# Kernel tuning notes

Measured on AMD Instinct MI355X. Metric: run time of the kernel, lower is better.

Reference implementation:

```python
import jax, jax.numpy as jnp
import numpy as np

IMG = 800.0
OUT = 7          # roi_size
SR = 2           # sampling_ratio per bin axis
STRIDES = (4, 8, 16)
N_CLASS = 21


def _make_rois(key, n):
    k1, k2, k3, k4 = jax.random.split(key, 4)
    cy = jax.random.uniform(k1, (n,), minval=100.0, maxval=700.0)
    cx = jax.random.uniform(k2, (n,), minval=100.0, maxval=700.0)
    # log-uniform sizes 32..448 px -> spans pyramid levels 2..4
    h = jnp.exp(jax.random.uniform(k3, (n,), minval=np.log(32.0), maxval=np.log(448.0)))
    w = jnp.exp(jax.random.uniform(k4, (n,), minval=np.log(32.0), maxval=np.log(448.0)))
    y1 = jnp.clip(cy - h / 2, 0.0, IMG - 2)
    x1 = jnp.clip(cx - w / 2, 0.0, IMG - 2)
    y2 = jnp.clip(cy + h / 2, y1 + 1.0, IMG - 1)
    x2 = jnp.clip(cx + w / 2, x1 + 1.0, IMG - 1)
    return jnp.stack([y1, x1, y2, x2], axis=1)  # [N,4] (y1,x1,y2,x2) as in source


def setup_inputs() -> dict:
    key = jax.random.key(0)
    ks = jax.random.split(key, 12)
    B, C, N = 2, 512, 512
    inp = {
        'feat2': jax.random.normal(ks[0], (B, C, 200, 200), jnp.float32),
        'feat3': jax.random.normal(ks[1], (B, C, 100, 100), jnp.float32),
        'feat4': jax.random.normal(ks[2], (B, C, 50, 50), jnp.float32),
        'rois': _make_rois(ks[3], N),
        'roi_indices': jax.random.randint(ks[4], (N,), 0, B, jnp.int32),
        'w_fc1': jax.random.normal(ks[5], (C * OUT * OUT, 4096), jnp.float32) * 0.01,
        'b_fc1': jnp.zeros((4096,), jnp.float32),
        'w_fc2': jax.random.normal(ks[6], (4096, 4096), jnp.float32) * 0.01,
        'b_fc2': jnp.zeros((4096,), jnp.float32),
        'w_loc': jax.random.normal(ks[7], (4096, N_CLASS * 4), jnp.float32) * 0.01,
        'b_loc': jnp.zeros((N_CLASS * 4,), jnp.float32),
        'w_score': jax.random.normal(ks[8], (4096, N_CLASS), jnp.float32) * 0.01,
        'b_score': jnp.zeros((N_CLASS,), jnp.float32),
    }
    return inp


def roi_align(feat, boxes, b_idx, scale):
    """feat [B,C,H,W]; boxes [N,4] x1,y1,x2,y2 in image coords -> [N,C,OUT,OUT]."""
    H, W = feat.shape[2], feat.shape[3]
    x1 = boxes[:, 0] * scale
    y1 = boxes[:, 1] * scale
    x2 = boxes[:, 2] * scale
    y2 = boxes[:, 3] * scale
    roi_w = jnp.maximum(x2 - x1, 1.0)
    roi_h = jnp.maximum(y2 - y1, 1.0)
    S = OUT * SR
    offs = (jnp.arange(S, dtype=feat.dtype) + 0.5) / (SR * OUT)  # fraction of roi extent
    ys = jnp.clip(y1[:, None] + roi_h[:, None] * offs, 0.0, H - 1.0)  # [N,S]
    xs = jnp.clip(x1[:, None] + roi_w[:, None] * offs, 0.0, W - 1.0)
    y0f = jnp.floor(ys); x0f = jnp.floor(xs)
    ly = ys - y0f; lx = xs - x0f
    y0 = y0f.astype(jnp.int32); x0 = x0f.astype(jnp.int32)
    y1i = jnp.minimum(y0 + 1, H - 1); x1i = jnp.minimum(x0 + 1, W - 1)
    b = b_idx[:, None, None]

    def g(yi, xi):  # -> [N,S,S,C]
        return feat[b, :, yi[:, :, None], xi[:, None, :]]

    wy0 = (1 - ly)[:, :, None, None]; wy1 = ly[:, :, None, None]
    wx0 = (1 - lx)[:, None, :, None]; wx1 = lx[:, None, :, None]
    val = (g(y0, x0) * wy0 * wx0 + g(y0, x1i) * wy0 * wx1
           + g(y1i, x0) * wy1 * wx0 + g(y1i, x1i) * wy1 * wx1)  # [N,S,S,C]
    N, C = boxes.shape[0], feat.shape[1]
    pooled = val.reshape(N, OUT, SR, OUT, SR, C).mean(axis=(2, 4))  # [N,OUT,OUT,C]
    return jnp.transpose(pooled, (0, 3, 1, 2))


def reference(feat2, feat3, feat4, rois, roi_indices, w_fc1, b_fc1, w_fc2, b_fc2,
              w_loc, b_loc, w_score, b_score):
    # pyramid level assignment (levels 2..4)
    roi_h = rois[:, 2] - rois[:, 0] + 1.0
    roi_w = rois[:, 3] - rois[:, 1] + 1.0
    lvl = jnp.round(jnp.log2(jnp.sqrt(roi_h * roi_w) / 224.0) + 4.0)
    lvl = jnp.clip(lvl, 2.0, 4.0).astype(jnp.int32)  # [N]

    boxes_xyxy = rois[:, jnp.array([1, 0, 3, 2])]  # (x1,y1,x2,y2)
    b_idx = roi_indices.astype(jnp.int32)

    p2 = roi_align(feat2, boxes_xyxy, b_idx, 1.0 / STRIDES[0])
    p3 = roi_align(feat3, boxes_xyxy, b_idx, 1.0 / STRIDES[1])
    p4 = roi_align(feat4, boxes_xyxy, b_idx, 1.0 / STRIDES[2])
    m = lvl[:, None, None, None]
    pooled = jnp.where(m == 2, p2, jnp.where(m == 3, p3, p4))  # [N,C,7,7]
    # (per-level split + sort-by-original-index in the source == original roi order)

    flat = pooled.reshape(pooled.shape[0], -1)  # [N, C*7*7]
    fc6 = jax.nn.relu(flat @ w_fc1 + b_fc1)
    fc7 = jax.nn.relu(fc6 @ w_fc2 + b_fc2)
    roi_cls_locs = fc7 @ w_loc + b_loc
    roi_scores = fc7 @ w_score + b_score
    return roi_cls_locs, roi_scores
```

## Files before the change

### kernel.cpp

```cpp
#include <hip/hip_runtime.h>
#include <hip/hip_bf16.h>

typedef __attribute__((ext_vector_type(4))) float  f32x4;
typedef __attribute__((ext_vector_type(2))) float  f32x2;
typedef __attribute__((ext_vector_type(4))) short  s16x4;
typedef __attribute__((ext_vector_type(8))) short  s16x8;
typedef __attribute__((ext_vector_type(8))) __bf16 v8bf;

__device__ __forceinline__ short f2bf(float f) {
    unsigned u = __builtin_bit_cast(unsigned, f);
    unsigned r = (u + 0x7fffu + ((u >> 16) & 1u)) >> 16;
    return (short)r;
}
__device__ __forceinline__ float bf2f(short s) {
    unsigned u = ((unsigned)(unsigned short)s) << 16;
    return __builtin_bit_cast(float, u);
}
__device__ __forceinline__ v8bf as_bf(s16x8 x) { return __builtin_bit_cast(v8bf, x); }

__global__ __launch_bounds__(256) void roi_pool_kernel(
    const float* __restrict__ feat2, const float* __restrict__ feat3,
    const float* __restrict__ feat4, const float* __restrict__ rois,
    const int* __restrict__ roi_idx, float* __restrict__ out) {
    const int r = blockIdx.x;
    const float y1r = rois[r*4+0], x1r = rois[r*4+1];
    const float y2r = rois[r*4+2], x2r = rois[r*4+3];
    const float rh = y2r - y1r + 1.0f, rw = x2r - x1r + 1.0f;
    float lvlf = rintf(log2f(sqrtf(rh*rw) / 224.0f) + 4.0f);
    lvlf = fminf(fmaxf(lvlf, 2.0f), 4.0f);
    const int lvl = (int)lvlf;
    const float* feat; int H; float scale;
    if (lvl == 2)      { feat = feat2; H = 200; scale = 0.25f;   }
    else if (lvl == 3) { feat = feat3; H = 100; scale = 0.125f;  }
    else               { feat = feat4; H = 50;  scale = 0.0625f; }
    const int W = H;
    const int b = roi_idx[r];

    const float x1 = x1r*scale, y1 = y1r*scale, x2 = x2r*scale, y2 = y2r*scale;
    const float roiw = fmaxf(x2 - x1, 1.0f), roih = fmaxf(y2 - y1, 1.0f);

    __shared__ int   sy0[14], sy1[14], sx0[14], sx1[14];
    __shared__ float sly[14], slx[14];
    const int t = threadIdx.x;
    if (t < 14) {
        float off = ((float)t + 0.5f) * (1.0f/14.0f);
        float ys = fminf(fmaxf(y1 + roih*off, 0.0f), (float)(H-1));
        float yf = floorf(ys);
        sy0[t] = (int)yf; sly[t] = ys - yf; sy1[t] = min((int)yf + 1, H-1);
    } else if (t < 28) {
        int j = t - 14;
        float off = ((float)j + 0.5f) * (1.0f/14.0f);
        float xs = fminf(fmaxf(x1 + roiw*off, 0.0f), (float)(W-1));
        float xf = floorf(xs);
        sx0[j] = (int)xf; slx[j] = xs - xf; sx1[j] = min((int)xf + 1, W-1);
    }
    __syncthreads();

    const float* fb = feat + (size_t)b * 512 * H * W;
    float* ob = out + (size_t)r * 25088;
    for (int idx = t; idx < 25088; idx += 256) {
        const int c = idx / 49, p = idx % 49;
        const int oy = p / 7, ox = p % 7;
        const float* fc = fb + (size_t)c * H * W;
        float acc = 0.0f;
        #pragma unroll
        for (int sy = 0; sy < 2; ++sy) {
            const int iy = oy*2 + sy;
            const int ya = sy0[iy], yb = sy1[iy];
            const float ly = sly[iy], wy0 = 1.0f - ly;
            const float* r0 = fc + (size_t)ya * W;
            const float* r1 = fc + (size_t)yb * W;
            #pragma unroll
            for (int sx = 0; sx < 2; ++sx) {
                const int ix = ox*2 + sx;
                const int xa = sx0[ix], xb = sx1[ix];
                const float lx = slx[ix], wx0 = 1.0f - lx;
                acc += r0[xa]*wy0*wx0 + r0[xb]*wy0*lx
                     + r1[xa]*ly*wx0  + r1[xb]*ly*lx;
            }
        }
        ob[idx] = acc * 0.25f;
    }
}

#define GKS 4
__global__ __launch_bounds__(512) void gemm_split_kernel(
    const float* __restrict__ A, const float* __restrict__ B,
    float* __restrict__ P, int K, int N, int ksub) {
    __shared__ unsigned short As_hi[4096], As_lo[4096], Bs_hi[4096], Bs_lo[4096];

    const int tid = threadIdx.x;
    const int m0 = blockIdx.y * 128;
    const int n0 = blockIdx.x * 128;
    const int k0base = blockIdx.z * ksub;
    const int nsteps = ksub >> 5;

    const int w    = tid >> 6;
    const int lane = tid & 63;
    const int wm   = w >> 1;
    const int wn   = w & 1;
    const int lr   = lane & 15;
    const int lg   = lane >> 4;

    f32x4 acc[2][4];
    #pragma unroll
    for (int i = 0; i < 2; ++i)
        #pragma unroll
        for (int j = 0; j < 4; ++j) acc[i][j] = f32x4{0.f, 0.f, 0.f, 0.f};

    const int a_m  = tid >> 3;
    const int a_kc = tid & 7;
    const int b_np = tid & 63;
    const int b_kq = tid >> 6;

    for (int step = 0; step < nsteps; ++step) {
        const int k0 = k0base + (step << 5);
        {
            const float* ap = A + (size_t)(m0 + a_m) * K + k0 + a_kc * 4;
            f32x4 v0 = *(const f32x4*)ap;
            f32x4 v1 = *(const f32x4*)(ap + (size_t)64 * K);
            const int kg = a_kc >> 1, sub0 = (a_kc & 1) * 4;
            const int e0 = (((kg << 10) + a_m * 8 + sub0) ^ (kg << 4));
            const int e1 = (((kg << 10) + (a_m + 64) * 8 + sub0) ^ (kg << 4));
            s16x4 h0, l0, h1, l1;
            #pragma unroll
            for (int j = 0; j < 4; ++j) {
                short h = f2bf(v0[j]); h0[j] = h; l0[j] = f2bf(v0[j] - bf2f(h));
                short g = f2bf(v1[j]); h1[j] = g; l1[j] = f2bf(v1[j] - bf2f(g));
            }
            *(s16x4*)(&As_hi[e0]) = h0; *(s16x4*)(&As_lo[e0]) = l0;
            *(s16x4*)(&As_hi[e1]) = h1; *(s16x4*)(&As_lo[e1]) = l1;
        }
        {
            const float* bp = B + (size_t)(k0 + b_kq * 4) * N + n0 + b_np * 2;
            f32x2 u0 = *(const f32x2*)bp;
            f32x2 u1 = *(const f32x2*)(bp + (size_t)N);
            f32x2 u2 = *(const f32x2*)(bp + (size_t)2 * N);
            f32x2 u3 = *(const f32x2*)(bp + (size_t)3 * N);
            const int kg = b_kq >> 1, sub0 = (b_kq & 1) * 4;
            #pragma unroll
            for (int e = 0; e < 2; ++e) {
                float vals[4] = {u0[e], u1[e], u2[e], u3[e]};
                s16x4 h, l;
                #pragma unroll
                for (int j = 0; j < 4; ++j) {
                    short hh = f2bf(vals[j]); h[j] = hh; l[j] = f2bf(vals[j] - bf2f(hh));
                }
                const int ei = (((kg << 10) + (b_np * 2 + e) * 8 + sub0) ^ (kg << 4));
                *(s16x4*)(&Bs_hi[ei]) = h; *(s16x4*)(&Bs_lo[ei]) = l;
            }
        }
        __syncthreads();
        s16x8 a_hi[2], a_lo[2];
        #pragma unroll
        for (int i = 0; i < 2; ++i) {
            const int m = wm * 32 + i * 16 + lr;
            const int e = (((lg << 10) + m * 8) ^ (lg << 4));
            a_hi[i] = *(const s16x8*)(&As_hi[e]);
            a_lo[i] = *(const s16x8*)(&As_lo[e]);
        }
        #pragma unroll
        for (int j = 0; j < 4; ++j) {
            const int n = wn * 64 + j * 16 + lr;
            const int e = (((lg << 10) + n * 8) ^ (lg << 4));
            v8bf b_hi = as_bf(*(const s16x8*)(&Bs_hi[e]));
            v8bf b_lo = as_bf(*(const s16x8*)(&Bs_lo[e]));
            #pragma unroll
            for (int i = 0; i < 2; ++i) {
                v8bf ah = as_bf(a_hi[i]), al = as_bf(a_lo[i]);
                acc[i][j] = __builtin_amdgcn_mfma_f32_16x16x32_bf16(ah, b_hi, acc[i][j], 0, 0, 0);
                acc[i][j] = __builtin_amdgcn_mfma_f32_16x16x32_bf16(ah, b_lo, acc[i][j], 0, 0, 0);
                acc[i][j] = __builtin_amdgcn_mfma_f32_16x16x32_bf16(al, b_hi, acc[i][j], 0, 0, 0);
            }
        }
        __syncthreads();
    }
    float* pb = P + (size_t)blockIdx.z * 512 * N;
    #pragma unroll
    for (int i = 0; i < 2; ++i)
        #pragma unroll
        for (int j = 0; j < 4; ++j) {
            const int gn = n0 + wn * 64 + j * 16 + lr;
            #pragma unroll
            for (int rr = 0; rr < 4; ++rr) {
                const int gm = m0 + wm * 32 + i * 16 + lg * 4 + rr;
                pb[(size_t)gm * N + gn] = acc[i][j][rr];
            }
        }
}

__global__ __launch_bounds__(256) void reduce_bias_relu(
    const float* __restrict__ P, const float* __restrict__ bias,
    float* __restrict__ out, int total, int N, int do_relu) {
    int i = (blockIdx.x * 256 + threadIdx.x) * 4;
    if (i >= total) return;
    f32x4 a0 = *(const f32x4*)(P + i);
    f32x4 a1 = *(const f32x4*)(P + (size_t)total + i);
    f32x4 a2 = *(const f32x4*)(P + (size_t)2 * total + i);
    f32x4 a3 = *(const f32x4*)(P + (size_t)3 * total + i);
    f32x4 bb = *(const f32x4*)(bias + (i % N));
    f32x4 r = (a0 + a1) + (a2 + a3) + bb;
    if (do_relu) {
        #pragma unroll
        for (int j = 0; j < 4; ++j) r[j] = fmaxf(r[j], 0.f);
    }
    *(f32x4*)(out + i) = r;
}

__global__ __launch_bounds__(128) void heads_kernel(
    const float* __restrict__ fc7,
    const float* __restrict__ w_loc, const float* __restrict__ b_loc,
    const float* __restrict__ w_score, const float* __restrict__ b_score,
    float* __restrict__ out, int nroi) {
    __shared__ float row[4096];
    const int r = blockIdx.x;
    const float* fr = fc7 + (size_t)r * 4096;
    for (int i = threadIdx.x; i < 4096; i += 128) row[i] = fr[i];
    __syncthreads();
    const int n = threadIdx.x;
    if (n < 84) {
        float s0 = 0.f, s1 = 0.f, s2 = 0.f, s3 = 0.f;
        for (int k = 0; k < 4096; k += 4) {
            s0 += row[k+0] * w_loc[(size_t)(k+0) * 84 + n];
            s1 += row[k+1] * w_loc[(size_t)(k+1) * 84 + n];
            s2 += row[k+2] * w_loc[(size_t)(k+2) * 84 + n];
            s3 += row[k+3] * w_loc[(size_t)(k+3) * 84 + n];
        }
        out[(size_t)r * 84 + n] = b_loc[n] + ((s0 + s1) + (s2 + s3));
    } else if (n < 105) {
        const int c = n - 84;
        float s0 = 0.f, s1 = 0.f, s2 = 0.f, s3 = 0.f;
        for (int k = 0; k < 4096; k += 4) {
            s0 += row[k+0] * w_score[(size_t)(k+0) * 21 + c];
            s1 += row[k+1] * w_score[(size_t)(k+1) * 21 + c];
            s2 += row[k+2] * w_score[(size_t)(k+2) * 21 + c];
            s3 += row[k+3] * w_score[(size_t)(k+3) * 21 + c];
        }
        out[(size_t)nroi * 84 + (size_t)r * 21 + c] = b_score[c] + ((s0 + s1) + (s2 + s3));
    }
}

extern "C" void kernel_launch(void* const* d_in, const int* in_sizes, int n_in,
                              void* d_out, int out_size, void* d_ws, size_t ws_size,
                              hipStream_t stream) {
    const float* feat2   = (const float*)d_in[0];
    const float* feat3   = (const float*)d_in[1];
    const float* feat4   = (const float*)d_in[2];
    const float* rois    = (const float*)d_in[3];
    const int*   roi_idx = (const int*)d_in[4];
    const float* w_fc1   = (const float*)d_in[5];
    const float* b_fc1   = (const float*)d_in[6];
    const float* w_fc2   = (const float*)d_in[7];
    const float* b_fc2   = (const float*)d_in[8];
    const float* w_loc   = (const float*)d_in[9];
    const float* b_loc   = (const float*)d_in[10];
    const float* w_score = (const float*)d_in[11];
    const float* b_score = (const float*)d_in[12];
    float* out = (float*)d_out;

    const int nroi = in_sizes[4];
    const int FDIM = 25088;
    const int HID  = 4096;

    char* ws = (char*)d_ws;
    const size_t off_flat = 0;
    const size_t off_part = 51380224;
    const size_t off_fc6  = off_part + 33554432;
    const size_t need     = off_fc6 + 8388608;
    if (ws_size < need) return;
    float* flat = (float*)(ws + off_flat);
    float* part = (float*)(ws + off_part);
    float* fc6  = (float*)(ws + off_fc6);
    float* fc7  = (float*)(ws + off_flat);

    roi_pool_kernel<<<nroi, 256, 0, stream>>>(feat2, feat3, feat4, rois, roi_idx, flat);

    gemm_split_kernel<<<dim3(HID/128, 512/128, GKS), 512, 0, stream>>>(
        flat, w_fc1, part, FDIM, HID, FDIM / GKS);
    reduce_bias_relu<<<(512 * HID / 4 + 255) / 256, 256, 0, stream>>>(
        part, b_fc1, fc6, 512 * HID, HID, 1);

    gemm_split_kernel<<<dim3(HID/128, 512/128, GKS), 512, 0, stream>>>(
        fc6, w_fc2, part, HID, HID, HID / GKS);
    reduce_bias_relu<<<(512 * HID / 4 + 255) / 256, 256, 0, stream>>>(
        part, b_fc2, fc7, 512 * HID, HID, 1);

    heads_kernel<<<nroi, 128, 0, stream>>>(fc7, w_loc, b_loc, w_score, b_score, out, nroi);
}
```

Baseline: 1.408 ms.

## Rewrite pipeline with pre-split bf16 activations, 256x256 double-buffered GEMM and atomic split-K

The ROI pool now writes activations already split into bf16 hi/lo planes in an MFMA-ready tiled layout, and the fc6 reduce does the same for the second GEMM. The GEMM uses 256x256 tiles with 8 K-splits and stages A into LDS directly via global_load_lds. It double-buffers A and B, overlaps the next B conversion with MFMAs, and accumulates split-K partials with atomicAdd into a zeroed buffer. The heads kernel splits K across two thread halves. These changes cut redundant A conversion and partial-buffer traffic, at the cost of fp32 atomics, which make the summation order nondeterministic, plus extra zeroing launches.

```diff
diff --git a/kernel.cpp b/kernel.cpp
--- a/kernel.cpp
+++ b/kernel.cpp
@@ -2,31 +2,35 @@
 #include <hip/hip_bf16.h>
 
 typedef __attribute__((ext_vector_type(4))) float  f32x4;
-typedef __attribute__((ext_vector_type(2))) float  f32x2;
-typedef __attribute__((ext_vector_type(4))) short  s16x4;
 typedef __attribute__((ext_vector_type(8))) short  s16x8;
 typedef __attribute__((ext_vector_type(8))) __bf16 v8bf;
 
-__device__ __forceinline__ short f2bf(float f) {
+__device__ __forceinline__ unsigned short f2bf_u(float f) {
     unsigned u = __builtin_bit_cast(unsigned, f);
     unsigned r = (u + 0x7fffu + ((u >> 16) & 1u)) >> 16;
-    return (short)r;
-}
-__device__ __forceinline__ float bf2f(short s) {
-    unsigned u = ((unsigned)(unsigned short)s) << 16;
+    return (unsigned short)r;
+}
+__device__ __forceinline__ float bfu2f(unsigned short s) {
+    unsigned u = ((unsigned)s) << 16;
     return __builtin_bit_cast(float, u);
 }
-__device__ __forceinline__ v8bf as_bf(s16x8 x) { return __builtin_bit_cast(v8bf, x); }
-
-__global__ __launch_bounds__(256) void roi_pool_kernel(
+
+__global__ __launch_bounds__(448) void roi_pool_split(
     const float* __restrict__ feat2, const float* __restrict__ feat3,
     const float* __restrict__ feat4, const float* __restrict__ rois,
-    const int* __restrict__ roi_idx, float* __restrict__ out) {
-    const int r = blockIdx.x;
+    const int* __restrict__ roi_idx,
+    unsigned short* __restrict__ Ah, unsigned short* __restrict__ Al) {
+    const int r  = blockIdx.x;
+    const int by = blockIdx.y;
+    const int t  = threadIdx.x;
+
+    __shared__ int   syA[14], syB[14], sxA[14], sxB[14];
+    __shared__ float sly[14], slx[14];
+    __shared__ float pool[3584];
+
     const float y1r = rois[r*4+0], x1r = rois[r*4+1];
     const float y2r = rois[r*4+2], x2r = rois[r*4+3];
-    const float rh = y2r - y1r + 1.0f, rw = x2r - x1r + 1.0f;
-    float lvlf = rintf(log2f(sqrtf(rh*rw) / 224.0f) + 4.0f);
+    float lvlf = rintf(log2f(sqrtf((y2r - y1r + 1.0f) * (x2r - x1r + 1.0f)) / 224.0f) + 4.0f);
     lvlf = fminf(fmaxf(lvlf, 2.0f), 4.0f);
     const int lvl = (int)lvlf;
     const float* feat; int H; float scale;
@@ -34,209 +38,281 @@
     else if (lvl == 3) { feat = feat3; H = 100; scale = 0.125f;  }
     else               { feat = feat4; H = 50;  scale = 0.0625f; }
     const int W = H;
-    const int b = roi_idx[r];
+    const int HW = H * W;
 
     const float x1 = x1r*scale, y1 = y1r*scale, x2 = x2r*scale, y2 = y2r*scale;
     const float roiw = fmaxf(x2 - x1, 1.0f), roih = fmaxf(y2 - y1, 1.0f);
 
-    __shared__ int   sy0[14], sy1[14], sx0[14], sx1[14];
-    __shared__ float sly[14], slx[14];
-    const int t = threadIdx.x;
     if (t < 14) {
         float off = ((float)t + 0.5f) * (1.0f/14.0f);
         float ys = fminf(fmaxf(y1 + roih*off, 0.0f), (float)(H-1));
         float yf = floorf(ys);
-        sy0[t] = (int)yf; sly[t] = ys - yf; sy1[t] = min((int)yf + 1, H-1);
+        int ya = (int)yf;
+        syA[t] = ya * W; sly[t] = ys - yf; syB[t] = min(ya + 1, H-1) * W;
     } else if (t < 28) {
         int j = t - 14;
         float off = ((float)j + 0.5f) * (1.0f/14.0f);
         float xs = fminf(fmaxf(x1 + roiw*off, 0.0f), (float)(W-1));
         float xf = floorf(xs);
-        sx0[j] = (int)xf; slx[j] = xs - xf; sx1[j] = min((int)xf + 1, W-1);
-    }
-    __syncthreads();
-
-    const float* fb = feat + (size_t)b * 512 * H * W;
-    float* ob = out + (size_t)r * 25088;
-    for (int idx = t; idx < 25088; idx += 256) {
-        const int c = idx / 49, p = idx % 49;
-        const int oy = p / 7, ox = p % 7;
-        const float* fc = fb + (size_t)c * H * W;
+        int xa = (int)xf;
+        sxA[j] = xa; slx[j] = xs - xf; sxB[j] = min(xa + 1, W-1);
+    }
+    __syncthreads();
+
+    const float* fb = feat + (size_t)roi_idx[r] * 512 * HW;
+    const int wv = t >> 6, lane = t & 63;
+
+    #pragma unroll
+    for (int j = 0; j < 8; ++j) {
+        const int kl = wv*512 + j*64 + lane;
+        const int kg = by*3584 + kl;
+        const int c  = kg / 49;
+        const int p  = kg - c*49;
+        const int oy = p / 7;
+        const int ox = p - oy*7;
+        const float* fc = fb + (size_t)c * HW;
         float acc = 0.0f;
         #pragma unroll
         for (int sy = 0; sy < 2; ++sy) {
             const int iy = oy*2 + sy;
-            const int ya = sy0[iy], yb = sy1[iy];
+            const int ra = syA[iy], rb = syB[iy];
             const float ly = sly[iy], wy0 = 1.0f - ly;
-            const float* r0 = fc + (size_t)ya * W;
-            const float* r1 = fc + (size_t)yb * W;
             #pragma unroll
             for (int sx = 0; sx < 2; ++sx) {
                 const int ix = ox*2 + sx;
-                const int xa = sx0[ix], xb = sx1[ix];
+                const int xa = sxA[ix], xb = sxB[ix];
                 const float lx = slx[ix], wx0 = 1.0f - lx;
-                acc += r0[xa]*wy0*wx0 + r0[xb]*wy0*lx
-                     + r1[xa]*ly*wx0  + r1[xb]*ly*lx;
+                acc += fc[ra+xa]*wy0*wx0 + fc[ra+xb]*wy0*lx
+                     + fc[rb+xa]*ly*wx0  + fc[rb+xb]*ly*lx;
             }
         }
-        ob[idx] = acc * 0.25f;
-    }
-}
-
-#define GKS 4
-__global__ __launch_bounds__(512) void gemm_split_kernel(
-    const float* __restrict__ A, const float* __restrict__ B,
-    float* __restrict__ P, int K, int N, int ksub) {
-    __shared__ unsigned short As_hi[4096], As_lo[4096], Bs_hi[4096], Bs_lo[4096];
-
-    const int tid = threadIdx.x;
-    const int m0 = blockIdx.y * 128;
-    const int n0 = blockIdx.x * 128;
-    const int k0base = blockIdx.z * ksub;
+        pool[kl] = acc * 0.25f;
+    }
+    __syncthreads();
+
+    const int k0l = t * 8;
+    const int k0  = by*3584 + k0l;
+    f32x4 v0 = *(const f32x4*)(&pool[k0l]);
+    f32x4 v1 = *(const f32x4*)(&pool[k0l+4]);
+    float v[8] = {v0[0],v0[1],v0[2],v0[3],v1[0],v1[1],v1[2],v1[3]};
+    s16x8 hi, lo;
+    #pragma unroll
+    for (int i = 0; i < 8; ++i) {
+        unsigned short h = f2bf_u(v[i]);
+        hi[i] = (short)h;
+        lo[i] = (short)f2bf_u(v[i] - bfu2f(h));
+    }
+    const int mb = r >> 4, row = r & 15;
+    const int kb = k0 >> 5, ko = (k0 >> 3) & 3;
+    const size_t off = ((((size_t)mb*784 + kb)*4 + ko)*16 + row)*8;
+    *(s16x8*)(Ah + off) = hi;
+    *(s16x8*)(Al + off) = lo;
+}
+
+__global__ __launch_bounds__(256) void zero_f32(float* __restrict__ p, int n4) {
+    int i = blockIdx.x*256 + threadIdx.x;
+    if (i < n4) ((f32x4*)p)[i] = f32x4{0.f,0.f,0.f,0.f};
+}
+
+__global__ __launch_bounds__(512, 2) void gemm_split3(
+    const unsigned short* __restrict__ Ah, const unsigned short* __restrict__ Al,
+    const float* __restrict__ B, float* __restrict__ P,
+    const int K, const int ksub) {
+    extern __shared__ char lds[];
+    const int tid  = threadIdx.x;
+    const int lane = tid & 63;
+    const int wv   = tid >> 6;
+    const int wm   = wv >> 2;
+    const int wn   = wv & 3;
+
+    int L = (int)blockIdx.x;
+    L = (L & 7) * 32 + (L >> 3);
+    const int mblk = L & 1;
+    const int nblk = (L >> 1) & 15;
+    const int zblk = L >> 5;
+    const int m0 = mblk * 256;
+    const int n0 = nblk * 256;
+    const int KB = K >> 5;
+    const int kb0 = (zblk * ksub) >> 5;
     const int nsteps = ksub >> 5;
 
-    const int w    = tid >> 6;
-    const int lane = tid & 63;
-    const int wm   = w >> 1;
-    const int wn   = w & 1;
-    const int lr   = lane & 15;
-    const int lg   = lane >> 4;
-
-    f32x4 acc[2][4];
-    #pragma unroll
-    for (int i = 0; i < 2; ++i)
-        #pragma unroll
-        for (int j = 0; j < 4; ++j) acc[i][j] = f32x4{0.f, 0.f, 0.f, 0.f};
-
-    const int a_m  = tid >> 3;
-    const int a_kc = tid & 7;
-    const int b_np = tid & 63;
-    const int b_kq = tid >> 6;
-
-    for (int step = 0; step < nsteps; ++step) {
-        const int k0 = k0base + (step << 5);
-        {
-            const float* ap = A + (size_t)(m0 + a_m) * K + k0 + a_kc * 4;
-            f32x4 v0 = *(const f32x4*)ap;
-            f32x4 v1 = *(const f32x4*)(ap + (size_t)64 * K);
-            const int kg = a_kc >> 1, sub0 = (a_kc & 1) * 4;
-            const int e0 = (((kg << 10) + a_m * 8 + sub0) ^ (kg << 4));
-            const int e1 = (((kg << 10) + (a_m + 64) * 8 + sub0) ^ (kg << 4));
-            s16x4 h0, l0, h1, l1;
+    const int b_col = tid & 15;
+    const int b_nb  = (tid >> 4) & 15;
+    const int b_kq  = tid >> 8;
+    const float* Bbase = B + (size_t)(n0 + b_nb*16 + b_col);
+
+    f32x4 acc[8][4];
+    #pragma unroll
+    for (int i = 0; i < 8; ++i)
+        #pragma unroll
+        for (int j = 0; j < 4; ++j) acc[i][j] = f32x4{0.f,0.f,0.f,0.f};
+
+    float bv[16];
+
+    auto loadB = [&](int kb) {
+        const float* bp = Bbase + (size_t)(kb*32 + b_kq*16) * 4096;
+        #pragma unroll
+        for (int i = 0; i < 16; ++i) bv[i] = bp[(size_t)i * 4096];
+    };
+    auto stageA = [&](int kb, char* buf) {
+        #pragma unroll
+        for (int c = 0; c < 4; ++c) {
+            const int ch = wv*4 + c;
+            const unsigned short* src = ((ch & 16) ? Al : Ah)
+                + ((size_t)((m0 >> 4) + (ch & 15)) * KB + kb) * 512 + lane*8;
+            char* dst = buf + (ch >> 4) * 16384 + (ch & 15) * 1024;
+            __builtin_amdgcn_global_load_lds((const void*)src, (void*)dst, 16, 0, 0);
+        }
+    };
+    auto convB = [&](char* buf) {
+        #pragma unroll
+        for (int o2 = 0; o2 < 2; ++o2) {
+            s16x8 hi, lo;
             #pragma unroll
-            for (int j = 0; j < 4; ++j) {
-                short h = f2bf(v0[j]); h0[j] = h; l0[j] = f2bf(v0[j] - bf2f(h));
-                short g = f2bf(v1[j]); h1[j] = g; l1[j] = f2bf(v1[j] - bf2f(g));
+            for (int i = 0; i < 8; ++i) {
+                float f = bv[o2*8 + i];
+                unsigned short h = f2bf_u(f);
+                hi[i] = (short)h;
+                lo[i] = (short)f2bf_u(f - bfu2f(h));
             }
-            *(s16x4*)(&As_hi[e0]) = h0; *(s16x4*)(&As_lo[e0]) = l0;
-            *(s16x4*)(&As_hi[e1]) = h1; *(s16x4*)(&As_lo[e1]) = l1;
-        }
-        {
-            const float* bp = B + (size_t)(k0 + b_kq * 4) * N + n0 + b_np * 2;
-            f32x2 u0 = *(const f32x2*)bp;
-            f32x2 u1 = *(const f32x2*)(bp + (size_t)N);
-            f32x2 u2 = *(const f32x2*)(bp + (size_t)2 * N);
-            f32x2 u3 = *(const f32x2*)(bp + (size_t)3 * N);
-            const int kg = b_kq >> 1, sub0 = (b_kq & 1) * 4;
+            const int oct = b_kq*2 + o2;
+            char* p = buf + 32768 + b_nb*1024 + oct*256 + b_col*16;
+            *(s16x8*)p = hi;
+            *(s16x8*)(p + 16384) = lo;
+        }
+    };
+    auto mfma_half = [&](int h, const char* buf) {
+        s16x8 ah[4], al[4];
+        #pragma unroll
+        for (int mf = 0; mf < 4; ++mf) {
+            const int ch = wm*8 + h*4 + mf;
+            ah[mf] = *(const s16x8*)(buf + ch*1024 + lane*16);
+            al[mf] = *(const s16x8*)(buf + 16384 + ch*1024 + lane*16);
+        }
+        #pragma unroll
+        for (int nf = 0; nf < 4; ++nf) {
+            const int nb = wn*4 + nf;
+            v8bf bh = __builtin_bit_cast(v8bf, *(const s16x8*)(buf + 32768 + nb*1024 + lane*16));
+            v8bf bl = __builtin_bit_cast(v8bf, *(const s16x8*)(buf + 49152 + nb*1024 + lane*16));
             #pragma unroll
-            for (int e = 0; e < 2; ++e) {
-                float vals[4] = {u0[e], u1[e], u2[e], u3[e]};
-                s16x4 h, l;
-                #pragma unroll
-                for (int j = 0; j < 4; ++j) {
-                    short hh = f2bf(vals[j]); h[j] = hh; l[j] = f2bf(vals[j] - bf2f(hh));
-                }
-                const int ei = (((kg << 10) + (b_np * 2 + e) * 8 + sub0) ^ (kg << 4));
-                *(s16x4*)(&Bs_hi[ei]) = h; *(s16x4*)(&Bs_lo[ei]) = l;
+            for (int mf = 0; mf < 4; ++mf) {
+                v8bf a1 = __builtin_bit_cast(v8bf, ah[mf]);
+                v8bf a2 = __builtin_bit_cast(v8bf, al[mf]);
+                const int mi = h*4 + mf;
+                acc[mi][nf] = __builtin_amdgcn_mfma_f32_16x16x32_bf16(a1, bh, acc[mi][nf], 0,0,0);
+                acc[mi][nf] = __builtin_amdgcn_mfma_f32_16x16x32_bf16(a1, bl, acc[mi][nf], 0,0,0);
+                acc[mi][nf] = __builtin_amdgcn_mfma_f32_16x16x32_bf16(a2, bh, acc[mi][nf], 0,0,0);
             }
         }
+    };
+
+    char* buf0 = lds;
+    char* buf1 = lds + 65536;
+
+    stageA(kb0, buf0);
+    loadB(kb0);
+    convB(buf0);
+    __syncthreads();
+
+    for (int s = 0; s < nsteps; ++s) {
+        char* cur = (s & 1) ? buf1 : buf0;
+        char* nxt = (s & 1) ? buf0 : buf1;
+        const bool more = (s + 1 < nsteps);
+        if (more) { stageA(kb0 + s + 1, nxt); loadB(kb0 + s + 1); }
+        mfma_half(0, cur);
+        if (more) convB(nxt);
+        mfma_half(1, cur);
         __syncthreads();
-        s16x8 a_hi[2], a_lo[2];
-        #pragma unroll
-        for (int i = 0; i < 2; ++i) {
-            const int m = wm * 32 + i * 16 + lr;
-            const int e = (((lg << 10) + m * 8) ^ (lg << 4));
-            a_hi[i] = *(const s16x8*)(&As_hi[e]);
-            a_lo[i] = *(const s16x8*)(&As_lo[e]);
-        }
-        #pragma unroll
-        for (int j = 0; j < 4; ++j) {
-            const int n = wn * 64 + j * 16 + lr;
-            const int e = (((lg << 10) + n * 8) ^ (lg << 4));
-            v8bf b_hi = as_bf(*(const s16x8*)(&Bs_hi[e]));
-            v8bf b_lo = as_bf(*(const s16x8*)(&Bs_lo[e]));
+    }
+
+    const int orow = (lane >> 4) * 4;
+    const int ocol = lane & 15;
+    #pragma unroll
+    for (int mi = 0; mi < 8; ++mi) {
+        const int gm = m0 + wm*128 + mi*16 + orow;
+        #pragma unroll
+        for (int nf = 0; nf < 4; ++nf) {
+            const int gn = n0 + wn*64 + nf*16 + ocol;
+            float* pp = P + (size_t)gm*4096 + gn;
             #pragma unroll
-            for (int i = 0; i < 2; ++i) {
-                v8bf ah = as_bf(a_hi[i]), al = as_bf(a_lo[i]);
-                acc[i][j] = __builtin_amdgcn_mfma_f32_16x16x32_bf16(ah, b_hi, acc[i][j], 0, 0, 0);
-                acc[i][j] = __builtin_amdgcn_mfma_f32_16x16x32_bf16(ah, b_lo, acc[i][j], 0, 0, 0);
-                acc[i][j] = __builtin_amdgcn_mfma_f32_16x16x32_bf16(al, b_hi, acc[i][j], 0, 0, 0);
-            }
-        }
-        __syncthreads();
-    }
-    float* pb = P + (size_t)blockIdx.z * 512 * N;
-    #pragma unroll
-    for (int i = 0; i < 2; ++i)
-        #pragma unroll
-        for (int j = 0; j < 4; ++j) {
-            const int gn = n0 + wn * 64 + j * 16 + lr;
-            #pragma unroll
-            for (int rr = 0; rr < 4; ++rr) {
-                const int gm = m0 + wm * 32 + i * 16 + lg * 4 + rr;
-                pb[(size_t)gm * N + gn] = acc[i][j][rr];
-            }
-        }
-}
-
-__global__ __launch_bounds__(256) void reduce_bias_relu(
+            for (int rr = 0; rr < 4; ++rr)
+                atomicAdd(pp + (size_t)rr*4096, acc[mi][nf][rr]);
+        }
+    }
+}
+
+__global__ __launch_bounds__(256) void reduce_split(
     const float* __restrict__ P, const float* __restrict__ bias,
-    float* __restrict__ out, int total, int N, int do_relu) {
-    int i = (blockIdx.x * 256 + threadIdx.x) * 4;
-    if (i >= total) return;
-    f32x4 a0 = *(const f32x4*)(P + i);
-    f32x4 a1 = *(const f32x4*)(P + (size_t)total + i);
-    f32x4 a2 = *(const f32x4*)(P + (size_t)2 * total + i);
-    f32x4 a3 = *(const f32x4*)(P + (size_t)3 * total + i);
-    f32x4 bb = *(const f32x4*)(bias + (i % N));
-    f32x4 r = (a0 + a1) + (a2 + a3) + bb;
-    if (do_relu) {
-        #pragma unroll
-        for (int j = 0; j < 4; ++j) r[j] = fmaxf(r[j], 0.f);
-    }
-    *(f32x4*)(out + i) = r;
-}
-
-__global__ __launch_bounds__(128) void heads_kernel(
+    unsigned short* __restrict__ Ah, unsigned short* __restrict__ Al) {
+    const int g = blockIdx.x*256 + threadIdx.x;
+    const int m = g >> 9;
+    const int k0 = (g & 511) * 8;
+    const float* pp = P + (size_t)m*4096 + k0;
+    f32x4 v0 = *(const f32x4*)pp, v1 = *(const f32x4*)(pp + 4);
+    f32x4 b0 = *(const f32x4*)(bias + k0), b1 = *(const f32x4*)(bias + k0 + 4);
+    float v[8];
+    #pragma unroll
+    for (int i = 0; i < 4; ++i) { v[i] = fmaxf(v0[i] + b0[i], 0.f); v[i+4] = fmaxf(v1[i] + b1[i], 0.f); }
+    s16x8 hi, lo;
+    #pragma unroll
+    for (int i = 0; i < 8; ++i) {
+        unsigned short h = f2bf_u(v[i]);
+        hi[i] = (short)h;
+        lo[i] = (short)f2bf_u(v[i] - bfu2f(h));
+    }
+    const int mb = m >> 4, row = m & 15;
+    const int kb = k0 >> 5, ko = (k0 >> 3) & 3;
+    const size_t off = ((((size_t)mb*128 + kb)*4 + ko)*16 + row)*8;
+    *(s16x8*)(Ah + off) = hi;
+    *(s16x8*)(Al + off) = lo;
+}
+
+__global__ __launch_bounds__(256) void reduce_bias_relu_f32(
+    const float* __restrict__ P, const float* __restrict__ bias,
+    float* __restrict__ out) {
+    const int g = blockIdx.x*256 + threadIdx.x;
+    const int m = g >> 9;
+    const int k0 = (g & 511) * 8;
+    const float* pp = P + (size_t)m*4096 + k0;
+    f32x4 v0 = *(const f32x4*)pp, v1 = *(const f32x4*)(pp + 4);
+    f32x4 b0 = *(const f32x4*)(bias + k0), b1 = *(const f32x4*)(bias + k0 + 4);
+    #pragma unroll
+    for (int i = 0; i < 4; ++i) { v0[i] = fmaxf(v0[i] + b0[i], 0.f); v1[i] = fmaxf(v1[i] + b1[i], 0.f); }
+    float* op = out + (size_t)m*4096 + k0;
+    *(f32x4*)op = v0;
+    *(f32x4*)(op + 4) = v1;
+}
+
+__global__ __launch_bounds__(256) void heads_kernel(
     const float* __restrict__ fc7,
     const float* __restrict__ w_loc, const float* __restrict__ b_loc,
     const float* __restrict__ w_score, const float* __restrict__ b_score,
     float* __restrict__ out, int nroi) {
     __shared__ float row[4096];
-    const int r = blockIdx.x;
+    __shared__ float part[105];
+    const int r = blockIdx.x, t = threadIdx.x;
     const float* fr = fc7 + (size_t)r * 4096;
-    for (int i = threadIdx.x; i < 4096; i += 128) row[i] = fr[i];
-    __syncthreads();
-    const int n = threadIdx.x;
-    if (n < 84) {
-        float s0 = 0.f, s1 = 0.f, s2 = 0.f, s3 = 0.f;
-        for (int k = 0; k < 4096; k += 4) {
-            s0 += row[k+0] * w_loc[(size_t)(k+0) * 84 + n];
-            s1 += row[k+1] * w_loc[(size_t)(k+1) * 84 + n];
-            s2 += row[k+2] * w_loc[(size_t)(k+2) * 84 + n];
-            s3 += row[k+3] * w_loc[(size_t)(k+3) * 84 + n];
-        }
-        out[(size_t)r * 84 + n] = b_loc[n] + ((s0 + s1) + (s2 + s3));
-    } else if (n < 105) {
-        const int c = n - 84;
-        float s0 = 0.f, s1 = 0.f, s2 = 0.f, s3 = 0.f;
-        for (int k = 0; k < 4096; k += 4) {
-            s0 += row[k+0] * w_score[(size_t)(k+0) * 21 + c];
-            s1 += row[k+1] * w_score[(size_t)(k+1) * 21 + c];
-            s2 += row[k+2] * w_score[(size_t)(k+2) * 21 + c];
-            s3 += row[k+3] * w_score[(size_t)(k+3) * 21 + c];
-        }
-        out[(size_t)nroi * 84 + (size_t)r * 21 + c] = b_score[c] + ((s0 + s1) + (s2 + s3));
+    for (int i = t; i < 4096; i += 256) row[i] = fr[i];
+    __syncthreads();
+    const bool active = t < 210;
+    int half = 0, c = 0;
+    float s = 0.f;
+    if (active) {
+        half = t / 105; c = t - half*105;
+        const float* wp; int ldw;
+        if (c < 84) { wp = w_loc + c; ldw = 84; }
+        else        { wp = w_score + (c - 84); ldw = 21; }
+        const int kb = half * 2048;
+        #pragma unroll 8
+        for (int k = 0; k < 2048; ++k)
+            s += row[kb + k] * wp[(size_t)(kb + k) * ldw];
+    }
+    if (active && half) part[c] = s;
+    __syncthreads();
+    if (active && !half) {
+        float o = s + part[c];
+        if (c < 84) out[(size_t)r*84 + c] = o + b_loc[c];
+        else        out[(size_t)nroi*84 + (size_t)r*21 + (c - 84)] = o + b_score[c - 84];
     }
 }
 
@@ -257,33 +333,36 @@
     const float* w_score = (const float*)d_in[11];
     const float* b_score = (const float*)d_in[12];
     float* out = (float*)d_out;
-
     const int nroi = in_sizes[4];
-    const int FDIM = 25088;
-    const int HID  = 4096;
 
     char* ws = (char*)d_ws;
-    const size_t off_flat = 0;
-    const size_t off_part = 51380224;
-    const size_t off_fc6  = off_part + 33554432;
-    const size_t need     = off_fc6 + 8388608;
+    const size_t off_A1h = 0;
+    const size_t off_A1l = 25690112;
+    const size_t off_P   = 51380224;
+    const size_t off_A2h = 59768832;
+    const size_t off_A2l = 63963136;
+    const size_t off_f7  = 68157440;
+    const size_t need    = 76546048;
     if (ws_size < need) return;
-    float* flat = (float*)(ws + off_flat);
-    float* part = (float*)(ws + off_part);
-    float* fc6  = (float*)(ws + off_fc6);
-    float* fc7  = (float*)(ws + off_flat);
-
-    roi_pool_kernel<<<nroi, 256, 0, stream>>>(feat2, feat3, feat4, rois, roi_idx, flat);
-
-    gemm_split_kernel<<<dim3(HID/128, 512/128, GKS), 512, 0, stream>>>(
-        flat, w_fc1, part, FDIM, HID, FDIM / GKS);
-    reduce_bias_relu<<<(512 * HID / 4 + 255) / 256, 256, 0, stream>>>(
-        part, b_fc1, fc6, 512 * HID, HID, 1);
-
-    gemm_split_kernel<<<dim3(HID/128, 512/128, GKS), 512, 0, stream>>>(
-        fc6, w_fc2, part, HID, HID, HID / GKS);
-    reduce_bias_relu<<<(512 * HID / 4 + 255) / 256, 256, 0, stream>>>(
-        part, b_fc2, fc7, 512 * HID, HID, 1);
-
-    heads_kernel<<<nroi, 128, 0, stream>>>(fc7, w_loc, b_loc, w_score, b_score, out, nroi);
-}
+    unsigned short* A1h = (unsigned short*)(ws + off_A1h);
+    unsigned short* A1l = (unsigned short*)(ws + off_A1l);
+    float*          P   = (float*)(ws + off_P);
+    unsigned short* A2h = (unsigned short*)(ws + off_A2h);
+    unsigned short* A2l = (unsigned short*)(ws + off_A2l);
+    float*          fc7 = (float*)(ws + off_f7);
+
+    hipFuncSetAttribute((const void*)gemm_split3,
+                        hipFuncAttributeMaxDynamicSharedMemorySize, 131072);
+
+    roi_pool_split<<<dim3(512, 7), 448, 0, stream>>>(feat2, feat3, feat4, rois, roi_idx, A1h, A1l);
+
+    zero_f32<<<2048, 256, 0, stream>>>(P, 524288);
+    gemm_split3<<<256, 512, 131072, stream>>>(A1h, A1l, w_fc1, P, 25088, 3136);
+    reduce_split<<<1024, 256, 0, stream>>>(P, b_fc1, A2h, A2l);
+
+    zero_f32<<<2048, 256, 0, stream>>>(P, 524288);
+    gemm_split3<<<256, 512, 131072, stream>>>(A2h, A2l, w_fc2, P, 4096, 512);
+    reduce_bias_relu_f32<<<1024, 256, 0, stream>>>(P, b_fc2, fc7);
+
+    heads_kernel<<<512, 256, 0, stream>>>(fc7, w_loc, b_loc, w_score, b_score, out, nroi);
+}
```

Result: faster. 1.271 ms (-9.7%).
